# Performance work log

Hardware: AMD Instinct MI355X
Metric: run time of the kernel (lower is better)

The kernel has to match this reference:

```python
import jax, jax.numpy as jnp
import numpy as np

Q_DIM = 9   # state(7) + action(2)
KV_DIM = 5  # fixed by get_input_tensors: 4 relative features + r_trans
H = 3
D = KV_DIM * H  # 15


def setup_inputs() -> dict:
    key = jax.random.key(0)
    ks = jax.random.split(key, 16)
    b, t = 32, 256

    def u(k, shape, fan_in):
        lim = (1.0 / fan_in) ** 0.5
        return jax.random.uniform(k, shape, jnp.float32, -lim, lim)

    return {
        "state": jax.random.normal(ks[0], (b, t, 7), jnp.float32),
        "action": jax.random.normal(ks[1], (b, t, 2), jnp.float32),
        "Wk": u(ks[2], (D, KV_DIM), KV_DIM),
        "Wq": u(ks[3], (D, Q_DIM), Q_DIM),
        "Wv": u(ks[4], (D, KV_DIM), KV_DIM),
        "att_bias": jax.random.uniform(ks[5], (KV_DIM,), jnp.float32, -0.1, 0.1),
        "Wscore": u(ks[6], (1, KV_DIM), KV_DIM),
        "bscore": u(ks[7], (1,), KV_DIM),
        "g1": jnp.ones((D,), jnp.float32),
        "beta1": jnp.zeros((D,), jnp.float32),
        "W1": u(ks[8], (5 * D, D), D),
        "bff1": u(ks[9], (5 * D,), D),
        "W2": u(ks[10], (D, 5 * D), 5 * D),
        "bff2": u(ks[11], (D,), 5 * D),
        "g2": jnp.ones((D,), jnp.float32),
        "beta2": jnp.zeros((D,), jnp.float32),
    }


def _layernorm(x, g, b, eps=1e-5):
    m = jnp.mean(x, axis=-1, keepdims=True)
    v = jnp.var(x, axis=-1, keepdims=True)
    return (x - m) * jax.lax.rsqrt(v + eps) * g + b


def _get_input_tensors(state):
    b, t, _ = state.shape
    init = state[..., :4]                                  # (b,t,4)
    rel = init[:, None, :, :] - init[:, :, None, :]        # (b,t,t,4): row i, col j -> s_j - s_i
    xy = rel.reshape(b, t, t, 2, 2).transpose(0, 1, 2, 4, 3)  # [...,0,:]=(x,vx), [...,1,:]=(y,vy)
    ang = -state[..., -1] + 0.5 * jnp.pi                   # (b,t)
    c = jnp.cos(ang)[:, None, :, None]                     # broadcast over row dim -> angle of col j
    s = jnp.sin(ang)[:, None, :, None]
    xr = xy[..., 0, :] * c - xy[..., 1, :] * s             # (b,t,t,2)
    yr = xy[..., 0, :] * s + xy[..., 1, :] * c
    rel = jnp.concatenate([xr, yr], axis=3)                # [xn,vxn,yn,vyn]
    rel = rel.reshape(b, t, t, 2, 2).transpose(0, 1, 2, 4, 3).reshape(b, t, t, 4)  # [xn,yn,vxn,vyn]
    # drop diagonal (j != i) via precomputed off-diagonal column indices
    rows = jnp.arange(t)[:, None]
    j = jnp.arange(t - 1)[None, :]
    cols = j + (j >= rows)                                 # (t,t-1)
    rel = rel[:, rows, cols, :]                            # (b,t,t-1,4)
    r = jnp.sqrt(rel[..., 0] ** 2 + rel[..., 1] ** 2)[..., None]  # (b,t,t-1,1)
    r_trans = 1.0 / (1.0 + jnp.exp(-1.0 + 5.0 * (r - 0.2)))
    kv_x = jnp.concatenate([rel[..., :2] / r, rel[..., 2:], r_trans], axis=-1)  # (b,t,t-1,5)
    return state, kv_x


def reference(state, action, Wk, Wq, Wv, att_bias, Wscore, bscore,
              g1, beta1, W1, bff1, W2, bff2, g2, beta2):
    q_x, kv_x = _get_input_tensors(state)
    q_x = jnp.concatenate([q_x, action], axis=-1)          # (b,t,Q_DIM)
    b, t, tm1, _ = kv_x.shape

    keys = (kv_x @ Wk.T).reshape(b, t, tm1, H, KV_DIM)     # (b,t,t-1,h,k)
    queries = (q_x @ Wq.T).reshape(b, t, 1, H, KV_DIM)
    e = jnp.tanh(keys + queries + att_bias)
    score = (e @ Wscore.T + bscore)[..., 0]                # (b,t,t-1,h)
    values = (kv_x @ Wv.T).reshape(b, t, tm1, H, KV_DIM)
    w = jax.nn.softmax(score, axis=2)                      # softmax over the t-1 neighbours
    x = jnp.einsum('btjh,btjhk->bthk', w, values).reshape(b, t, H * KV_DIM)

    x = _layernorm(x, g1, beta1)
    y = jax.nn.relu(x @ W1.T + bff1) @ W2.T + bff2
    x = x + y
    return _layernorm(x, g2, beta2)
```

## Files before the change

### kernel.cpp

```cpp
#include <hip/hip_runtime.h>
#include <math.h>

#define TT   256
#define TM1  255
#define QD   9
#define KD   5
#define NH   3
#define DD   15
#define HID  75
#define NR   18

#define K2E  2.8853900817779268f
#define L2E  1.4426950408889634f
#define INVK 0.34657359027997264f

typedef float v2f __attribute__((ext_vector_type(2)));

__device__ __forceinline__ v2f v2splat(float s) { v2f r; r.x = s; r.y = s; return r; }

__device__ __forceinline__ float fast_rcp(float x) {
    return __builtin_amdgcn_rcpf(x);
}

__device__ __forceinline__ float exp2_raw(float x) {
    float r; asm("v_exp_f32 %0, %1" : "=v"(r) : "v"(x)); return r;
}

template<int CTRL>
__device__ __forceinline__ float dpp_add(float x) {
    int y = __builtin_amdgcn_update_dpp(0, __float_as_int(x), CTRL, 0xf, 0xf, true);
    return x + __int_as_float(y);
}

__device__ __forceinline__ float wave_sum63(float x) {
    x = dpp_add<0x111>(x);
    x = dpp_add<0x112>(x);
    x = dpp_add<0x114>(x);
    x = dpp_add<0x118>(x);
    x = dpp_add<0x142>(x);
    x = dpp_add<0x143>(x);
    return x;
}

__device__ __forceinline__ float bcast(float x, int l) {
    return __int_as_float(__builtin_amdgcn_readlane(__float_as_int(x), l));
}

__global__ __launch_bounds__(256)
void fused_block_kernel(const float* __restrict__ state,
                        const float* __restrict__ action,
                        const float* __restrict__ Wk,
                        const float* __restrict__ Wq,
                        const float* __restrict__ Wv,
                        const float* __restrict__ att_bias,
                        const float* __restrict__ Wscore,
                        const float* __restrict__ bscore,
                        const float* __restrict__ g1,
                        const float* __restrict__ beta1,
                        const float* __restrict__ W1,
                        const float* __restrict__ bff1,
                        const float* __restrict__ W2,
                        const float* __restrict__ bff2,
                        const float* __restrict__ g2,
                        const float* __restrict__ beta2,
                        float* __restrict__ out)
{
    const int tid  = threadIdx.x;
    const int lane = tid & 63;
    const int wv   = __builtin_amdgcn_readfirstlane(tid >> 6);
    const int qgrp = blockIdx.x * 4 + wv;
    const int b    = qgrp >> 8;
    const int qi   = qgrp & 255;

    __shared__ float s_h[4][76];

    const float* __restrict__ sb  = state + (size_t)b*TT*7;
    const float* __restrict__ sti = sb + qi*7;
    const float si0 = sti[0], si1 = sti[1], si2 = sti[2], si3 = sti[3];

    float qv = 0.0f;
    if (lane < DD) {
        float acc = att_bias[lane % KD];
        #pragma unroll
        for (int k = 0; k < 7; k++) acc = fmaf(Wq[lane*QD+k], sti[k], acc);
        acc = fmaf(Wq[lane*QD+7], action[((size_t)b*TT+qi)*2 + 0], acc);
        acc = fmaf(Wq[lane*QD+8], action[((size_t)b*TT+qi)*2 + 1], acc);
        qv = acc * K2E;
    }
    float qb2[DD];
    #pragma unroll
    for (int d = 0; d < DD; d++) qb2[d] = bcast(qv, d);

    float w2[KD];
    float Cn = bscore[0];
    #pragma unroll
    for (int kk = 0; kk < KD; kk++) { float w = Wscore[kk]; w2[kk] = -K2E*w; Cn += w; }
    const float C2 = L2E * Cn;

    v2f rv[NR];
    #pragma unroll
    for (int n = 0; n < NR; n++) rv[n] = v2splat(0.0f);

    #pragma unroll
    for (int g = 0; g < 2; g++) {
        const int mm0 = lane + g*128;
        const int mm1 = mm0 + 64;
        const int jj0 = mm0 + (mm0 >= qi ? 1 : 0);
        int       jj1 = mm1 + (mm1 >= qi ? 1 : 0);
        jj1 = (jj1 < TT) ? jj1 : (TT-1);
        const float* __restrict__ r0 = sb + jj0*7;
        const float* __restrict__ r1 = sb + jj1*7;

        v2f d0, d1, d2, d3, th;
        d0.x = r0[0]; d0.y = r1[0];
        d1.x = r0[1]; d1.y = r1[1];
        d2.x = r0[2]; d2.y = r1[2];
        d3.x = r0[3]; d3.y = r1[3];
        th.x = r0[6]; th.y = r1[6];
        d0 = d0 - v2splat(si0);
        d1 = d1 - v2splat(si1);
        d2 = d2 - v2splat(si2);
        d3 = d3 - v2splat(si3);

        v2f cs, sn;
        cs.x = __sinf(th.x); cs.y = __sinf(th.y);
        sn.x = __cosf(th.x); sn.y = __cosf(th.y);

        v2f xr0 = d0*cs - d1*sn;
        v2f yr0 = d0*sn + d1*cs;
        v2f xr1 = d2*cs - d3*sn;
        v2f yr1 = d2*sn + d3*cs;
        v2f s2  = xr0*xr0 + yr0*yr0;
        s2.x = fmaxf(s2.x, 1e-12f);
        s2.y = fmaxf(s2.y, 1e-12f);
        v2f rinv;
        rinv.x = __builtin_amdgcn_rsqf(s2.x);
        rinv.y = __builtin_amdgcn_rsqf(s2.y);
        v2f r = s2 * rinv;
        v2f ea;
        ea.x = exp2_raw(fmaf(7.213475204444817f, r.x, -2.8853900817779268f));
        ea.y = exp2_raw(fmaf(7.213475204444817f, r.y, -2.8853900817779268f));
        v2f rt;
        rt.x = fast_rcp(1.0f + ea.x);
        rt.y = fast_rcp(1.0f + ea.y);

        v2f t  = v2splat(K2E) * rinv;
        v2f f0 = t * xr0;
        v2f f1 = t * yr0;
        v2f f2 = v2splat(K2E) * xr1;
        v2f f3 = v2splat(K2E) * yr1;
        v2f f4 = v2splat(K2E) * rt;

        v2f Cp;
        Cp.x = (mm0 < TM1) ? C2 : -100.0f;
        Cp.y = (mm1 < TM1) ? C2 : -100.0f;

        #pragma unroll
        for (int h = 0; h < NH; h++) {
            v2f sc = Cp;
            #pragma unroll
            for (int kk = 0; kk < KD; kk++) {
                const int d = h*KD + kk;
                v2f a = v2splat(qb2[d]);
                a = a + v2splat(Wk[d*KD+0]) * f0;
                a = a + v2splat(Wk[d*KD+1]) * f1;
                a = a + v2splat(Wk[d*KD+2]) * f2;
                a = a + v2splat(Wk[d*KD+3]) * f3;
                a = a + v2splat(Wk[d*KD+4]) * f4;
                v2f e;
                e.x = exp2_raw(a.x);
                e.y = exp2_raw(a.y);
                v2f sg;
                sg.x = fast_rcp(e.x + 1.0f);
                sg.y = fast_rcp(e.y + 1.0f);
                sc = sc + v2splat(w2[kk]) * sg;
            }
            v2f p;
            p.x = exp2_raw(sc.x);
            p.y = exp2_raw(sc.y);
            rv[h] = rv[h] + p;
            rv[NH+h*KD+0] = rv[NH+h*KD+0] + p * f0;
            rv[NH+h*KD+1] = rv[NH+h*KD+1] + p * f1;
            rv[NH+h*KD+2] = rv[NH+h*KD+2] + p * f2;
            rv[NH+h*KD+3] = rv[NH+h*KD+3] + p * f3;
            rv[NH+h*KD+4] = rv[NH+h*KD+4] + p * f4;
        }
    }

    float red[NR];
    #pragma unroll
    for (int n = 0; n < NR; n++) red[n] = rv[n].x + rv[n].y;
    #pragma unroll
    for (int n = 0; n < NR; n++) red[n] = wave_sum63(red[n]);
    float fin[NR];
    #pragma unroll
    for (int n = 0; n < NR; n++) fin[n] = bcast(red[n], 63);

    float xm = 0.0f;
    if (lane < DD) {
        const int h = lane / KD;
        float acc = 0.0f;
        #pragma unroll
        for (int c = 0; c < KD; c++) acc = fmaf(Wv[lane*KD+c], fin[NH+h*KD+c], acc);
        xm = acc * fast_rcp(fin[h]) * INVK;
    }

    float s1 = xm, sq = xm*xm;
    #pragma unroll
    for (int off = 8; off >= 1; off >>= 1) {
        s1 += __shfl_xor(s1, off, 16);
        sq += __shfl_xor(sq, off, 16);
    }
    const float mu1   = s1 * (1.0f/DD);
    const float rstd1 = rsqrtf(sq * (1.0f/DD) - mu1*mu1 + 1e-5f);
    float xln = 0.0f;
    if (lane < DD) xln = (xm - mu1) * rstd1 * g1[lane] + beta1[lane];

    float xs[DD];
    #pragma unroll
    for (int d = 0; d < DD; d++) xs[d] = bcast(xln, d);

    {
        float h0 = bff1[lane];
        #pragma unroll
        for (int k = 0; k < DD; k++) h0 = fmaf(W1[lane*DD+k], xs[k], h0);
        s_h[wv][lane] = fmaxf(h0, 0.0f);
        if (lane < HID-64) {
            float h1 = bff1[lane+64];
            #pragma unroll
            for (int k = 0; k < DD; k++) h1 = fmaf(W1[(lane+64)*DD+k], xs[k], h1);
            s_h[wv][lane+64] = fmaxf(h1, 0.0f);
        }
    }

    const int c2  = lane >> 4;
    const int d2c = lane & 15;
    const int cc  = (c2 < 3) ? c2 : 2;
    const int dc  = (d2c < DD) ? d2c : 0;
    float acc2 = 0.0f;
    #pragma unroll
    for (int k = 0; k < 25; k++)
        acc2 = fmaf(W2[dc*HID + cc*25 + k], s_h[wv][cc*25 + k], acc2);
    acc2 = (c2 < 3) ? acc2 : 0.0f;
    acc2 += __shfl_xor(acc2, 16);
    acc2 += __shfl_xor(acc2, 32);

    float x2 = 0.0f;
    if (lane < DD) x2 = xln + bff2[lane] + acc2;
    float t1 = x2, t2 = x2*x2;
    #pragma unroll
    for (int off = 8; off >= 1; off >>= 1) {
        t1 += __shfl_xor(t1, off, 16);
        t2 += __shfl_xor(t2, off, 16);
    }
    const float mu2   = t1 * (1.0f/DD);
    const float rstd2 = rsqrtf(t2 * (1.0f/DD) - mu2*mu2 + 1e-5f);
    if (lane < DD)
        out[(size_t)qgrp*DD + lane] = (x2 - mu2) * rstd2 * g2[lane] + beta2[lane];
}

extern "C" void kernel_launch(void* const* d_in, const int* in_sizes, int n_in,
                              void* d_out, int out_size, void* d_ws, size_t ws_size,
                              hipStream_t stream) {
    const float* state    = (const float*)d_in[0];
    const float* action   = (const float*)d_in[1];
    const float* Wk       = (const float*)d_in[2];
    const float* Wq       = (const float*)d_in[3];
    const float* Wv       = (const float*)d_in[4];
    const float* att_bias = (const float*)d_in[5];
    const float* Wscore   = (const float*)d_in[6];
    const float* bscore   = (const float*)d_in[7];
    const float* g1       = (const float*)d_in[8];
    const float* beta1    = (const float*)d_in[9];
    const float* W1       = (const float*)d_in[10];
    const float* bff1     = (const float*)d_in[11];
    const float* W2       = (const float*)d_in[12];
    const float* bff2     = (const float*)d_in[13];
    const float* g2       = (const float*)d_in[14];
    const float* beta2    = (const float*)d_in[15];
    float* out = (float*)d_out;

    dim3 grid(32 * 256 / 4);
    dim3 block(256);
    fused_block_kernel<<<grid, block, 0, stream>>>(
        state, action, Wk, Wq, Wv, att_bias, Wscore, bscore,
        g1, beta1, W1, bff1, W2, bff2, g2, beta2, out);
}
```

Baseline: 24.98 us.

## Stage batch state, precomputed sin/cos, and FFN weights in LDS

Each block cooperatively loads the batch's 256 state rows into shared memory as split arrays, with sin/cos of the angle computed once per row. W1 and W2 are staged into shared memory too. The attention loop then reads neighbour features from LDS instead of strided global loads, and skips repeating the trig per query. This costs a block-wide barrier and about 17KB of extra LDS per block, which may reduce occupancy.

Measured after the change: 25.72 us. +3.0%, slower.

```diff
diff --git a/kernel.cpp b/kernel.cpp
--- a/kernel.cpp
+++ b/kernel.cpp
@@ -9,6 +9,8 @@
 #define DD   15
 #define HID  75
 #define NR   18
+#define W1N  (HID*DD)
+#define W2N  (DD*HID)
 
 #define K2E  2.8853900817779268f
 #define L2E  1.4426950408889634f
@@ -72,12 +74,30 @@
     const int b    = qgrp >> 8;
     const int qi   = qgrp & 255;
 
+    __shared__ float s_s0[TT], s_s1[TT], s_s2[TT], s_s3[TT], s_sn[TT], s_cs[TT];
+    __shared__ float s_w1[W1N];
+    __shared__ float s_w2[W2N];
     __shared__ float s_h[4][76];
 
-    const float* __restrict__ sb  = state + (size_t)b*TT*7;
+    const float* __restrict__ sb = state + (size_t)b*TT*7;
+
+    {
+        const float* sj = sb + tid*7;
+        const float th = sj[6];
+        s_s0[tid] = sj[0];
+        s_s1[tid] = sj[1];
+        s_s2[tid] = sj[2];
+        s_s3[tid] = sj[3];
+        s_cs[tid] = __sinf(th);
+        s_sn[tid] = __cosf(th);
+    }
+    #pragma unroll
+    for (int i = tid; i < W1N; i += 256) s_w1[i] = W1[i];
+    #pragma unroll
+    for (int i = tid; i < W2N; i += 256) s_w2[i] = W2[i];
+
     const float* __restrict__ sti = sb + qi*7;
     const float si0 = sti[0], si1 = sti[1], si2 = sti[2], si3 = sti[3];
-
     float qv = 0.0f;
     if (lane < DD) {
         float acc = att_bias[lane % KD];
@@ -91,11 +111,13 @@
     #pragma unroll
     for (int d = 0; d < DD; d++) qb2[d] = bcast(qv, d);
 
-    float w2[KD];
+    float w2c[KD];
     float Cn = bscore[0];
     #pragma unroll
-    for (int kk = 0; kk < KD; kk++) { float w = Wscore[kk]; w2[kk] = -K2E*w; Cn += w; }
+    for (int kk = 0; kk < KD; kk++) { float w = Wscore[kk]; w2c[kk] = -K2E*w; Cn += w; }
     const float C2 = L2E * Cn;
+
+    __syncthreads();
 
     v2f rv[NR];
     #pragma unroll
@@ -108,23 +130,18 @@
         const int jj0 = mm0 + (mm0 >= qi ? 1 : 0);
         int       jj1 = mm1 + (mm1 >= qi ? 1 : 0);
         jj1 = (jj1 < TT) ? jj1 : (TT-1);
-        const float* __restrict__ r0 = sb + jj0*7;
-        const float* __restrict__ r1 = sb + jj1*7;
-
-        v2f d0, d1, d2, d3, th;
-        d0.x = r0[0]; d0.y = r1[0];
-        d1.x = r0[1]; d1.y = r1[1];
-        d2.x = r0[2]; d2.y = r1[2];
-        d3.x = r0[3]; d3.y = r1[3];
-        th.x = r0[6]; th.y = r1[6];
+
+        v2f d0, d1, d2, d3, cs, sn;
+        d0.x = s_s0[jj0]; d0.y = s_s0[jj1];
+        d1.x = s_s1[jj0]; d1.y = s_s1[jj1];
+        d2.x = s_s2[jj0]; d2.y = s_s2[jj1];
+        d3.x = s_s3[jj0]; d3.y = s_s3[jj1];
+        cs.x = s_cs[jj0]; cs.y = s_cs[jj1];
+        sn.x = s_sn[jj0]; sn.y = s_sn[jj1];
         d0 = d0 - v2splat(si0);
         d1 = d1 - v2splat(si1);
         d2 = d2 - v2splat(si2);
         d3 = d3 - v2splat(si3);
-
-        v2f cs, sn;
-        cs.x = __sinf(th.x); cs.y = __sinf(th.y);
-        sn.x = __cosf(th.x); sn.y = __cosf(th.y);
 
         v2f xr0 = d0*cs - d1*sn;
         v2f yr0 = d0*sn + d1*cs;
@@ -173,7 +190,7 @@
                 v2f sg;
                 sg.x = fast_rcp(e.x + 1.0f);
                 sg.y = fast_rcp(e.y + 1.0f);
-                sc = sc + v2splat(w2[kk]) * sg;
+                sc = sc + v2splat(w2c[kk]) * sg;
             }
             v2f p;
             p.x = exp2_raw(sc.x);
@@ -223,12 +240,12 @@
     {
         float h0 = bff1[lane];
         #pragma unroll
-        for (int k = 0; k < DD; k++) h0 = fmaf(W1[lane*DD+k], xs[k], h0);
+        for (int k = 0; k < DD; k++) h0 = fmaf(s_w1[lane*DD+k], xs[k], h0);
         s_h[wv][lane] = fmaxf(h0, 0.0f);
         if (lane < HID-64) {
             float h1 = bff1[lane+64];
             #pragma unroll
-            for (int k = 0; k < DD; k++) h1 = fmaf(W1[(lane+64)*DD+k], xs[k], h1);
+            for (int k = 0; k < DD; k++) h1 = fmaf(s_w1[(lane+64)*DD+k], xs[k], h1);
             s_h[wv][lane+64] = fmaxf(h1, 0.0f);
         }
     }
@@ -240,7 +257,7 @@
     float acc2 = 0.0f;
     #pragma unroll
     for (int k = 0; k < 25; k++)
-        acc2 = fmaf(W2[dc*HID + cc*25 + k], s_h[wv][cc*25 + k], acc2);
+        acc2 = fmaf(s_w2[dc*HID + cc*25 + k], s_h[wv][cc*25 + k], acc2);
     acc2 = (c2 < 3) ? acc2 : 0.0f;
     acc2 += __shfl_xor(acc2, 16);
     acc2 += __shfl_xor(acc2, 32);
```

## Stage Wk and score weights in LDS and interleave both neighbour groups

Applied to the files above, without the earlier changes.

Copies Wk plus the scaled score weights into a padded shared-memory table so each weight row loads as one float4 plus one float2, where before they were scalar global loads. The attention loop is reordered to compute features for both neighbour groups first, then loop over heads, reusing each weight load for both groups. This exposes more independent transcendental work per iteration. The cost is more live registers for the stored features and an added block barrier.

Result: no change. 24.94 us (-0.1%).

```diff
diff --git a/kernel.cpp b/kernel.cpp
--- a/kernel.cpp
+++ b/kernel.cpp
@@ -72,11 +72,20 @@
     const int b    = qgrp >> 8;
     const int qi   = qgrp & 255;
 
+    __shared__ __align__(16) float s_wk8[DD*8];
     __shared__ float s_h[4][76];
 
     const float* __restrict__ sb  = state + (size_t)b*TT*7;
     const float* __restrict__ sti = sb + qi*7;
     const float si0 = sti[0], si1 = sti[1], si2 = sti[2], si3 = sti[3];
+
+    if (tid < DD) {
+        #pragma unroll
+        for (int c = 0; c < KD; c++) s_wk8[tid*8+c] = Wk[tid*KD+c];
+        s_wk8[tid*8+5] = -K2E * Wscore[tid % KD];
+        s_wk8[tid*8+6] = 0.0f;
+        s_wk8[tid*8+7] = 0.0f;
+    }
 
     float qv = 0.0f;
     if (lane < DD) {
@@ -91,16 +100,14 @@
     #pragma unroll
     for (int d = 0; d < DD; d++) qb2[d] = bcast(qv, d);
 
-    float w2[KD];
     float Cn = bscore[0];
     #pragma unroll
-    for (int kk = 0; kk < KD; kk++) { float w = Wscore[kk]; w2[kk] = -K2E*w; Cn += w; }
+    for (int kk = 0; kk < KD; kk++) Cn += Wscore[kk];
     const float C2 = L2E * Cn;
 
-    v2f rv[NR];
-    #pragma unroll
-    for (int n = 0; n < NR; n++) rv[n] = v2splat(0.0f);
-
+    __syncthreads();
+
+    v2f F0[2], F1[2], F2[2], F3[2], F4[2], Cp[2];
     #pragma unroll
     for (int g = 0; g < 2; g++) {
         const int mm0 = lane + g*128;
@@ -145,46 +152,60 @@
         rt.y = fast_rcp(1.0f + ea.y);
 
         v2f t  = v2splat(K2E) * rinv;
-        v2f f0 = t * xr0;
-        v2f f1 = t * yr0;
-        v2f f2 = v2splat(K2E) * xr1;
-        v2f f3 = v2splat(K2E) * yr1;
-        v2f f4 = v2splat(K2E) * rt;
-
-        v2f Cp;
-        Cp.x = (mm0 < TM1) ? C2 : -100.0f;
-        Cp.y = (mm1 < TM1) ? C2 : -100.0f;
-
-        #pragma unroll
-        for (int h = 0; h < NH; h++) {
-            v2f sc = Cp;
-            #pragma unroll
-            for (int kk = 0; kk < KD; kk++) {
-                const int d = h*KD + kk;
-                v2f a = v2splat(qb2[d]);
-                a = a + v2splat(Wk[d*KD+0]) * f0;
-                a = a + v2splat(Wk[d*KD+1]) * f1;
-                a = a + v2splat(Wk[d*KD+2]) * f2;
-                a = a + v2splat(Wk[d*KD+3]) * f3;
-                a = a + v2splat(Wk[d*KD+4]) * f4;
-                v2f e;
-                e.x = exp2_raw(a.x);
-                e.y = exp2_raw(a.y);
-                v2f sg;
-                sg.x = fast_rcp(e.x + 1.0f);
-                sg.y = fast_rcp(e.y + 1.0f);
-                sc = sc + v2splat(w2[kk]) * sg;
-            }
-            v2f p;
-            p.x = exp2_raw(sc.x);
-            p.y = exp2_raw(sc.y);
-            rv[h] = rv[h] + p;
-            rv[NH+h*KD+0] = rv[NH+h*KD+0] + p * f0;
-            rv[NH+h*KD+1] = rv[NH+h*KD+1] + p * f1;
-            rv[NH+h*KD+2] = rv[NH+h*KD+2] + p * f2;
-            rv[NH+h*KD+3] = rv[NH+h*KD+3] + p * f3;
-            rv[NH+h*KD+4] = rv[NH+h*KD+4] + p * f4;
+        F0[g] = t * xr0;
+        F1[g] = t * yr0;
+        F2[g] = v2splat(K2E) * xr1;
+        F3[g] = v2splat(K2E) * yr1;
+        F4[g] = v2splat(K2E) * rt;
+
+        Cp[g].x = (mm0 < TM1) ? C2 : -100.0f;
+        Cp[g].y = (mm1 < TM1) ? C2 : -100.0f;
+    }
+
+    v2f rv[NR];
+    #pragma unroll
+    for (int n = 0; n < NR; n++) rv[n] = v2splat(0.0f);
+
+    #pragma unroll
+    for (int h = 0; h < NH; h++) {
+        v2f sc0 = Cp[0], sc1 = Cp[1];
+        #pragma unroll
+        for (int kk = 0; kk < KD; kk++) {
+            const int d = h*KD + kk;
+            const float4 wA = *(const float4*)&s_wk8[d*8];
+            const float2 wB = *(const float2*)&s_wk8[d*8+4];
+            const float qd = qb2[d];
+
+            v2f a0 = v2splat(qd);
+            a0 = a0 + v2splat(wA.x) * F0[0];
+            a0 = a0 + v2splat(wA.y) * F1[0];
+            a0 = a0 + v2splat(wA.z) * F2[0];
+            a0 = a0 + v2splat(wA.w) * F3[0];
+            a0 = a0 + v2splat(wB.x) * F4[0];
+            v2f a1 = v2splat(qd);
+            a1 = a1 + v2splat(wA.x) * F0[1];
+            a1 = a1 + v2splat(wA.y) * F1[1];
+            a1 = a1 + v2splat(wA.z) * F2[1];
+            a1 = a1 + v2splat(wA.w) * F3[1];
+            a1 = a1 + v2splat(wB.x) * F4[1];
+
+            v2f e0, e1, sg0, sg1;
+            e0.x = exp2_raw(a0.x); e0.y = exp2_raw(a0.y);
+            e1.x = exp2_raw(a1.x); e1.y = exp2_raw(a1.y);
+            sg0.x = fast_rcp(e0.x + 1.0f); sg0.y = fast_rcp(e0.y + 1.0f);
+            sg1.x = fast_rcp(e1.x + 1.0f); sg1.y = fast_rcp(e1.y + 1.0f);
+            sc0 = sc0 + v2splat(wB.y) * sg0;
+            sc1 = sc1 + v2splat(wB.y) * sg1;
         }
+        v2f p0, p1;
+        p0.x = exp2_raw(sc0.x); p0.y = exp2_raw(sc0.y);
+        p1.x = exp2_raw(sc1.x); p1.y = exp2_raw(sc1.y);
+        rv[h] = rv[h] + p0 + p1;
+        rv[NH+h*KD+0] = rv[NH+h*KD+0] + p0 * F0[0] + p1 * F0[1];
+        rv[NH+h*KD+1] = rv[NH+h*KD+1] + p0 * F1[0] + p1 * F1[1];
+        rv[NH+h*KD+2] = rv[NH+h*KD+2] + p0 * F2[0] + p1 * F2[1];
+        rv[NH+h*KD+3] = rv[NH+h*KD+3] + p0 * F3[0] + p1 * F3[1];
+        rv[NH+h*KD+4] = rv[NH+h*KD+4] + p0 * F4[0] + p1 * F4[1];
     }
 
     float red[NR];
```
